# Kernel optimization log

Measured on AMD Instinct MI355X. Metric: run time of the kernel, lower is better.

The kernel has to match this reference:

```python
import jax, jax.numpy as jnp
import numpy as np
import math

D_MODEL = 1024
N_HEADS = 16
D_K = D_MODEL // N_HEADS
B, S = 4, 2048


def setup_inputs() -> dict:
    key = jax.random.key(0)
    ks = jax.random.split(key, 11)
    std = 1.0 / math.sqrt(D_MODEL)
    inp = {
        "query": jax.random.normal(ks[0], (B, S, D_MODEL), dtype=jnp.float32),
        "key_in": jax.random.normal(ks[1], (B, S, D_MODEL), dtype=jnp.float32),
        "value": jax.random.normal(ks[2], (B, S, D_MODEL), dtype=jnp.float32),
        "Wq": jax.random.normal(ks[3], (D_MODEL, D_MODEL), dtype=jnp.float32) * std,
        "bq": jnp.zeros((D_MODEL,), dtype=jnp.float32),
        "Wk": jax.random.normal(ks[4], (D_MODEL, D_MODEL), dtype=jnp.float32) * std,
        "bk": jnp.zeros((D_MODEL,), dtype=jnp.float32),
        "Wv": jax.random.normal(ks[5], (D_MODEL, D_MODEL), dtype=jnp.float32) * std,
        "bv": jnp.zeros((D_MODEL,), dtype=jnp.float32),
        "Wo": jax.random.normal(ks[6], (D_MODEL, D_MODEL), dtype=jnp.float32) * std,
        "bo": jnp.zeros((D_MODEL,), dtype=jnp.float32),
    }
    return inp


def reference(query, key_in, value, Wq, bq, Wk, bk, Wv, bv, Wo, bo):
    b, s, _ = query.shape
    scale = math.sqrt(D_K)
    # projections: nn.Linear computes x @ W.T + b
    Q = (query @ Wq.T + bq).reshape(b, s, N_HEADS, D_K).transpose(0, 2, 1, 3)
    K = (key_in @ Wk.T + bk).reshape(b, s, N_HEADS, D_K).transpose(0, 2, 1, 3)
    V = (value @ Wv.T + bv).reshape(b, s, N_HEADS, D_K).transpose(0, 2, 1, 3)
    # [b, h, s, s]
    scores = jnp.einsum("bhqd,bhkd->bhqk", Q, K) / scale
    causal = jnp.tril(jnp.ones((s, s), dtype=bool))
    scores = jnp.where(causal[None, None, :, :], scores, jnp.float32(-1e9))
    attn = jax.nn.softmax(scores, axis=-1)
    out = jnp.einsum("bhqk,bhkd->bhqd", attn, V)
    out = out.transpose(0, 2, 1, 3).reshape(b, s, D_MODEL)
    return out @ Wo.T + bo
```

## Files before the change

kernel.cpp:

```cpp
#include <hip/hip_runtime.h>
#include <hip/hip_bf16.h>
#include <cstdint>

#define DM   1024
#define NH   16
#define DKK  64
#define BB   4
#define SS   2048

typedef __attribute__((ext_vector_type(8)))  short short8;
typedef __attribute__((ext_vector_type(4)))  float f32x4;
typedef __attribute__((ext_vector_type(16))) float f32x16;

__device__ __forceinline__ unsigned short f2bf(float f) {
    union { float f; uint32_t u; } v; v.f = f;
    uint32_t u = v.u;
    uint32_t r = (u + 0x7FFFu + ((u >> 16) & 1u)) >> 16;
    return (unsigned short)r;
}

__global__ void cvt_w(const float4* __restrict__ wq, const float4* __restrict__ wk,
                      const float4* __restrict__ wv, const float4* __restrict__ wo,
                      ushort4* __restrict__ dst)
{
    const int NW = 262144;
    int i = blockIdx.x * 256 + threadIdx.x;
    int a = i >> 18, off = i & (NW - 1);
    const float4* s = (a == 0 ? wq : a == 1 ? wk : a == 2 ? wv : wo) + off;
    float4 f = *s;
    ushort4 o;
    o.x = f2bf(f.x); o.y = f2bf(f.y); o.z = f2bf(f.z); o.w = f2bf(f.w);
    dst[i] = o;
}

__global__ void gemm_qkv(const float* __restrict__ Aq,
                         const float* __restrict__ Ak,
                         const float* __restrict__ Av,
                         const unsigned short* __restrict__ Wq,
                         const unsigned short* __restrict__ Wk,
                         const unsigned short* __restrict__ Wv,
                         const float* __restrict__ bq,
                         const float* __restrict__ bk,
                         const float* __restrict__ bv,
                         unsigned short* __restrict__ Qo,
                         unsigned short* __restrict__ Ko,
                         unsigned short* __restrict__ Vo,
                         const float qscale)
{
    const int orig = blockIdx.z * 512 + blockIdx.y * 8 + blockIdx.x;
    const int wid  = (orig & 7) * 192 + (orig >> 3);
    const int z    = wid >> 9;
    const int rem  = wid & 511;
    const int brow = (rem >> 3) * 128;
    const int bcol = (rem & 7) * 128;

    const float* A           = (z == 0) ? Aq : (z == 1) ? Ak : Av;
    const unsigned short* Bw = (z == 0) ? Wq : (z == 1) ? Wk : Wv;
    const float* bias        = (z == 0) ? bq : (z == 1) ? bk : bv;

    __shared__ unsigned short lA[128 * 64];
    __shared__ unsigned short lB[128 * 64];
    const int tid = threadIdx.x;
    const int w = tid >> 6, l = tid & 63;
    const int wr = (w >> 1) * 64, wc = (w & 1) * 64;
    const int lrow = l & 15;
    const int lk = (l >> 4) * 8;
    const int sr = l >> 3;
    const int sc = (l & 7) * 8;
    f32x4 acc[4][4] = {};

    for (int k0 = 0; k0 < 1024; k0 += 64) {
#pragma unroll
        for (int i = 0; i < 4; ++i) {
            const int chunk = w * 4 + i;
            const int r = chunk * 8 + sr;
            const unsigned short* gb = Bw + (size_t)(bcol + r) * 1024 + k0 + sc;
            __builtin_amdgcn_global_load_lds((__attribute__((address_space(1))) void*)gb,
                                             (__attribute__((address_space(3))) void*)(lB + chunk * 512),
                                             16, 0, 0);
        }
#pragma unroll
        for (int i = 0; i < 4; ++i) {
            const int chunk = w * 4 + i;
            const int r = chunk * 8 + sr;
            const float* ga = A + (size_t)(brow + r) * 1024 + k0 + sc;
            float4 f0 = *(const float4*)(ga);
            float4 f1 = *(const float4*)(ga + 4);
            union { uint32_t u[4]; short8 s8; } c;
            asm("v_cvt_pk_bf16_f32 %0, %1, %2" : "=v"(c.u[0]) : "v"(f0.x), "v"(f0.y));
            asm("v_cvt_pk_bf16_f32 %0, %1, %2" : "=v"(c.u[1]) : "v"(f0.z), "v"(f0.w));
            asm("v_cvt_pk_bf16_f32 %0, %1, %2" : "=v"(c.u[2]) : "v"(f1.x), "v"(f1.y));
            asm("v_cvt_pk_bf16_f32 %0, %1, %2" : "=v"(c.u[3]) : "v"(f1.z), "v"(f1.w));
            *(short8*)((char*)lA + chunk * 1024 + sr * 128 + sc * 2) = c.s8;
        }
        asm volatile("s_waitcnt vmcnt(0)" ::: "memory");
        __syncthreads();
#pragma unroll
        for (int kk = 0; kk < 2; ++kk) {
            short8 af[4], bfr[4];
#pragma unroll
            for (int m = 0; m < 4; ++m)
                af[m] = *(const short8*)(lA + (wr + m * 16 + lrow) * 64 + kk * 32 + lk);
#pragma unroll
            for (int n = 0; n < 4; ++n)
                bfr[n] = *(const short8*)(lB + (wc + n * 16 + lrow) * 64 + kk * 32 + lk);
#pragma unroll
            for (int m = 0; m < 4; ++m)
#pragma unroll
                for (int n = 0; n < 4; ++n)
                    acc[m][n] = __builtin_amdgcn_mfma_f32_16x16x32_bf16(af[m], bfr[n], acc[m][n], 0, 0, 0);
        }
        __syncthreads();
    }

    const float ascale = (z == 0) ? qscale : 1.0f;
#pragma unroll
    for (int m = 0; m < 4; ++m) {
#pragma unroll
        for (int n = 0; n < 4; ++n) {
            const int i0 = brow + wr + m * 16 + (l >> 4) * 4;
            const int j  = bcol + wc + n * 16 + lrow;
            const float bj = bias[j];
            const int hh = j >> 6, d = j & 63;
            if (z < 2) {
                unsigned short* Cb = (z == 0) ? Qo : Ko;
#pragma unroll
                for (int t = 0; t < 4; ++t) {
                    const int i = i0 + t;
                    const int b = i >> 11, s = i & 2047;
                    Cb[(((size_t)(b * NH + hh) * SS) + s) * DKK + d] = f2bf((acc[m][n][t] + bj) * ascale);
                }
            } else {
                const int b = i0 >> 11, s0 = i0 & 2047;
                ushort4 pk;
                pk.x = f2bf(acc[m][n][0] + bj);
                pk.y = f2bf(acc[m][n][1] + bj);
                pk.z = f2bf(acc[m][n][2] + bj);
                pk.w = f2bf(acc[m][n][3] + bj);
                *(ushort4*)(Vo + (((size_t)(b * NH + hh) * DKK) + d) * SS + s0) = pk;
            }
        }
    }
}

__global__ void gemm_out(const unsigned short* __restrict__ A,
                         const unsigned short* __restrict__ Bw,
                         const float* __restrict__ bias,
                         float* __restrict__ Cout)
{
    const int orig = blockIdx.y * 8 + blockIdx.x;
    const int wid  = (orig & 7) * 64 + (orig >> 3);
    const int brow = (wid >> 3) * 128;
    const int bcol = (wid & 7) * 128;

    __shared__ unsigned short lA[128 * 64];
    __shared__ unsigned short lB[128 * 64];
    const int tid = threadIdx.x;
    const int w = tid >> 6, l = tid & 63;
    const int wr = (w >> 1) * 64, wc = (w & 1) * 64;
    const int lrow = l & 15;
    const int lk = (l >> 4) * 8;
    const int sr = l >> 3;
    const int sc = (l & 7) * 8;
    f32x4 acc[4][4] = {};

    for (int k0 = 0; k0 < 1024; k0 += 64) {
#pragma unroll
        for (int i = 0; i < 4; ++i) {
            const int chunk = w * 4 + i;
            const int r = chunk * 8 + sr;
            const unsigned short* ga = A  + (size_t)(brow + r) * 1024 + k0 + sc;
            const unsigned short* gb = Bw + (size_t)(bcol + r) * 1024 + k0 + sc;
            __builtin_amdgcn_global_load_lds((__attribute__((address_space(1))) void*)ga,
                                             (__attribute__((address_space(3))) void*)(lA + chunk * 512),
                                             16, 0, 0);
            __builtin_amdgcn_global_load_lds((__attribute__((address_space(1))) void*)gb,
                                             (__attribute__((address_space(3))) void*)(lB + chunk * 512),
                                             16, 0, 0);
        }
        asm volatile("s_waitcnt vmcnt(0)" ::: "memory");
        __syncthreads();
#pragma unroll
        for (int kk = 0; kk < 2; ++kk) {
            short8 af[4], bfr[4];
#pragma unroll
            for (int m = 0; m < 4; ++m)
                af[m] = *(const short8*)(lA + (wr + m * 16 + lrow) * 64 + kk * 32 + lk);
#pragma unroll
            for (int n = 0; n < 4; ++n)
                bfr[n] = *(const short8*)(lB + (wc + n * 16 + lrow) * 64 + kk * 32 + lk);
#pragma unroll
            for (int m = 0; m < 4; ++m)
#pragma unroll
                for (int n = 0; n < 4; ++n)
                    acc[m][n] = __builtin_amdgcn_mfma_f32_16x16x32_bf16(af[m], bfr[n], acc[m][n], 0, 0, 0);
        }
        __syncthreads();
    }

#pragma unroll
    for (int m = 0; m < 4; ++m) {
#pragma unroll
        for (int n = 0; n < 4; ++n) {
            const int i0 = brow + wr + m * 16 + (l >> 4) * 4;
            const int j  = bcol + wc + n * 16 + lrow;
            const float bj = bias[j];
#pragma unroll
            for (int t = 0; t < 4; ++t)
                Cout[(size_t)(i0 + t) * DM + j] = acc[m][n][t] + bj;
        }
    }
}

__global__ __launch_bounds__(256) void attn_kernel(
        const unsigned short* __restrict__ Q,
        const unsigned short* __restrict__ K,
        const unsigned short* __restrict__ Vt,
        unsigned short* __restrict__ AO)
{
    const int flat = blockIdx.y * 16 + blockIdx.x;
    const int r8 = flat & 7, k8 = flat >> 3;
    const int bh = r8 * 8 + (k8 & 7);
    const int qchunk = 15 - (k8 >> 3);
    const int tid = threadIdx.x;
    const int w = tid >> 6, l = tid & 63;
    const int ln = l & 31, h = l >> 5;
    const int qb = qchunk * 128;
    const int q0w = qb + w * 32;

    __shared__ __align__(16) char lK[2][4096];
    __shared__ __align__(16) char lV[2][4096];

    const unsigned short* Qp = Q  + ((size_t)bh * SS + q0w) * DKK;
    const unsigned short* Kp = K  + (size_t)bh * SS * DKK;
    const unsigned short* Vp = Vt + (size_t)bh * DKK * SS;

    const int srow = tid >> 3, scb = tid & 7;
    const int swb = srow * 128 + ((scb * 16) ^ ((srow & 7) << 4));
    const unsigned short* ksrc = Kp + srow * DKK + scb * 8;
    const int vd = (scb < 4) ? srow : (srow + 32);
    const unsigned short* vsrc = Vp + (size_t)vd * SS + (scb & 3) * 8;

    int ka[4], va[4];
#pragma unroll
    for (int ks = 0; ks < 4; ++ks)
        ka[ks] = ln * 128 + ((ks * 32 + h * 16) ^ ((ln & 7) << 4));
#pragma unroll
    for (int c = 0; c < 4; ++c)
        va[c] = ln * 128 + ((c * 32 + h * 16) ^ ((ln & 7) << 4));

    short8 qf[4];
#pragma unroll
    for (int ks = 0; ks < 4; ++ks)
        qf[ks] = *(const short8*)(Qp + (size_t)ln * DKK + ks * 16 + h * 8);

    f32x16 o0 = {}, o1 = {};
    float lsum = 0.f;

    const int Tc = qb / 32;
    const int NT = Tc + 4;

    auto compute = [&](int t, int buf) {
        const char* kb = lK[buf];
        const char* vb = lV[buf];
        short8 kf[4];
#pragma unroll
        for (int ks = 0; ks < 4; ++ks) kf[ks] = *(const short8*)(kb + ka[ks]);

        f32x16 s = {};
        __builtin_amdgcn_s_setprio(1);
#pragma unroll
        for (int ks = 0; ks < 4; ++ks)
            s = __builtin_amdgcn_mfma_f32_32x32x16_bf16(kf[ks], qf[ks], s, 0, 0, 0);
        __builtin_amdgcn_s_setprio(0);

        const bool diag = (t == Tc + w);
#pragma unroll
        for (int r = 0; r < 16; ++r) {
            float e;
            asm("v_exp_f32 %0, %1" : "=v"(e) : "v"(s[r]));
            if (diag) {
                const int crow = (r & 3) + 8 * (r >> 2) + 4 * h;
                e = (crow > ln) ? 0.f : e;
            }
            s[r] = e;
            lsum += e;
        }

        uint32_t pk[8];
#pragma unroll
        for (int i = 0; i < 8; ++i) {
            uint32_t d;
            asm("v_cvt_pk_bf16_f32 %0, %1, %2" : "=v"(d) : "v"(s[2 * i]), "v"(s[2 * i + 1]));
            pk[i] = d;
        }
        asm("v_permlane32_swap_b32 %0, %1" : "+v"(pk[0]), "+v"(pk[2]));
        asm("v_permlane32_swap_b32 %0, %1" : "+v"(pk[1]), "+v"(pk[3]));
        asm("v_permlane32_swap_b32 %0, %1" : "+v"(pk[4]), "+v"(pk[6]));
        asm("v_permlane32_swap_b32 %0, %1" : "+v"(pk[5]), "+v"(pk[7]));

        union Ux { uint32_t u[4]; short8 s8; } pa0, pa1;
        pa0.u[0] = pk[0]; pa0.u[1] = pk[1]; pa0.u[2] = pk[2]; pa0.u[3] = pk[3];
        pa1.u[0] = pk[4]; pa1.u[1] = pk[5]; pa1.u[2] = pk[6]; pa1.u[3] = pk[7];

        short8 vf00 = *(const short8*)(vb + va[0]);
        short8 vf10 = *(const short8*)(vb + va[1]);
        short8 vf01 = *(const short8*)(vb + va[2]);
        short8 vf11 = *(const short8*)(vb + va[3]);

        __builtin_amdgcn_s_setprio(1);
        o0 = __builtin_amdgcn_mfma_f32_32x32x16_bf16(pa0.s8, vf00, o0, 0, 0, 0);
        o0 = __builtin_amdgcn_mfma_f32_32x32x16_bf16(pa1.s8, vf10, o0, 0, 0, 0);
        o1 = __builtin_amdgcn_mfma_f32_32x32x16_bf16(pa0.s8, vf01, o1, 0, 0, 0);
        o1 = __builtin_amdgcn_mfma_f32_32x32x16_bf16(pa1.s8, vf11, o1, 0, 0, 0);
        __builtin_amdgcn_s_setprio(0);
    };

    short8 kA = *(const short8*)(ksrc);
    short8 vA = *(const short8*)(vsrc);
    *(short8*)(&lK[0][swb]) = kA;
    *(short8*)(&lV[0][swb]) = vA;
    kA = *(const short8*)(ksrc + 2048);
    vA = *(const short8*)(vsrc + 32);
    short8 kB = {}, vB = {};
    __syncthreads();

    int t = 0, buf = 0;
    for (;;) {
        if (t + 2 < NT) {
            kB = *(const short8*)(ksrc + (size_t)(t + 2) * 2048);
            vB = *(const short8*)(vsrc + (size_t)(t + 2) * 32);
        }
        if (t <= Tc + w) compute(t, buf);
        if (t + 1 < NT) {
            *(short8*)(&lK[buf ^ 1][swb]) = kA;
            *(short8*)(&lV[buf ^ 1][swb]) = vA;
        }
        __syncthreads();
        buf ^= 1;
        if (++t == NT) break;

        if (t + 2 < NT) {
            kA = *(const short8*)(ksrc + (size_t)(t + 2) * 2048);
            vA = *(const short8*)(vsrc + (size_t)(t + 2) * 32);
        }
        if (t <= Tc + w) compute(t, buf);
        if (t + 1 < NT) {
            *(short8*)(&lK[buf ^ 1][swb]) = kB;
            *(short8*)(&lV[buf ^ 1][swb]) = vB;
        }
        __syncthreads();
        buf ^= 1;
        if (++t == NT) break;
    }

    lsum += __shfl_xor(lsum, 32, 64);
    const float rcp = 1.0f / lsum;

    const int bb = bh >> 4, hh = bh & 15;
#pragma unroll
    for (int r = 0; r < 16; ++r) {
        const int crow = (r & 3) + 8 * (r >> 2) + 4 * h;
        const float rl = __shfl(rcp, crow, 64);
        const size_t row = (size_t)(bb * SS + q0w + crow) * DM + hh * DKK;
        AO[row + ln]      = f2bf(o0[r] * rl);
        AO[row + 32 + ln] = f2bf(o1[r] * rl);
    }
}

extern "C" void kernel_launch(void* const* d_in, const int* in_sizes, int n_in,
                              void* d_out, int out_size, void* d_ws, size_t ws_size,
                              hipStream_t stream)
{
    const float* query  = (const float*)d_in[0];
    const float* key_in = (const float*)d_in[1];
    const float* value  = (const float*)d_in[2];
    const float* Wq = (const float*)d_in[3];
    const float* bq = (const float*)d_in[4];
    const float* Wk = (const float*)d_in[5];
    const float* bk = (const float*)d_in[6];
    const float* Wv = (const float*)d_in[7];
    const float* bv = (const float*)d_in[8];
    const float* Wo = (const float*)d_in[9];
    const float* bo = (const float*)d_in[10];

    const size_t NACT = (size_t)BB * SS * DM;
    const size_t NWT  = (size_t)DM * DM;

    unsigned short* ws  = (unsigned short*)d_ws;
    unsigned short* wqb = ws;
    unsigned short* wkb = wqb + NWT;
    unsigned short* wvb = wkb + NWT;
    unsigned short* wob = wvb + NWT;
    unsigned short* Qb  = wob + NWT;
    unsigned short* Kb  = Qb + NACT;
    unsigned short* Vtb = Kb + NACT;
    unsigned short* AOb = Vtb + NACT;

    const int n4 = (int)(4 * (NWT / 4));
    cvt_w<<<n4 / 256, 256, 0, stream>>>((const float4*)Wq, (const float4*)Wk,
                                        (const float4*)Wv, (const float4*)Wo,
                                        (ushort4*)ws);

    const float QSCALE = 0.125f * 1.44269504088896f;
    dim3 gq(DM / 128, (BB * SS) / 128, 3);
    gemm_qkv<<<gq, 256, 0, stream>>>(query, key_in, value, wqb, wkb, wvb,
                                     bq, bk, bv, Qb, Kb, Vtb, QSCALE);

    attn_kernel<<<dim3(16, 64), 256, 0, stream>>>(Qb, Kb, Vtb, AOb);

    dim3 gg(DM / 128, (BB * SS) / 128);
    gemm_out<<<gg, 256, 0, stream>>>(AOb, wob, bo, (float*)d_out);
}
```

Measured before the change: 175.2 us.

## Software-pipeline QKV GEMM with register-prefetched A, double-buffered B, swizzled LDS

The QKV projection GEMM now prefetches the next K-tile of fp32 activations into registers and the next weight tile into a second LDS buffer while computing the current tile. Raw barriers with partial vmcnt waits and s_setprio replace the full drain. The weight conversion kernel pre-swizzles bf16 weights so LDS reads use an XOR pattern that avoids bank conflicts, and the output GEMM's B reads use the same swizzle. This aims to hide global-load latency and cut LDS bank conflicts, at the cost of more LDS and registers, which may lower occupancy.

```diff
diff --git a/kernel.cpp b/kernel.cpp
--- a/kernel.cpp
+++ b/kernel.cpp
@@ -19,33 +19,37 @@
     return (unsigned short)r;
 }
 
-__global__ void cvt_w(const float4* __restrict__ wq, const float4* __restrict__ wk,
-                      const float4* __restrict__ wv, const float4* __restrict__ wo,
-                      ushort4* __restrict__ dst)
+#define GLL(src, dst) __builtin_amdgcn_global_load_lds(                      \
+        (__attribute__((address_space(1))) void*)(src),                      \
+        (__attribute__((address_space(3))) void*)(dst), 16, 0, 0)
+
+__global__ void cvt_w(const float* __restrict__ wq, const float* __restrict__ wk,
+                      const float* __restrict__ wv, const float* __restrict__ wo,
+                      unsigned short* __restrict__ dst)
 {
-    const int NW = 262144;
     int i = blockIdx.x * 256 + threadIdx.x;
-    int a = i >> 18, off = i & (NW - 1);
-    const float4* s = (a == 0 ? wq : a == 1 ? wk : a == 2 ? wv : wo) + off;
-    float4 f = *s;
-    ushort4 o;
-    o.x = f2bf(f.x); o.y = f2bf(f.y); o.z = f2bf(f.z); o.w = f2bf(f.w);
-    dst[i] = o;
-}
-
-__global__ void gemm_qkv(const float* __restrict__ Aq,
-                         const float* __restrict__ Ak,
-                         const float* __restrict__ Av,
-                         const unsigned short* __restrict__ Wq,
-                         const unsigned short* __restrict__ Wk,
-                         const unsigned short* __restrict__ Wv,
-                         const float* __restrict__ bq,
-                         const float* __restrict__ bk,
-                         const float* __restrict__ bv,
-                         unsigned short* __restrict__ Qo,
-                         unsigned short* __restrict__ Ko,
-                         unsigned short* __restrict__ Vo,
-                         const float qscale)
+    int a = i >> 17;
+    int r = i & 131071;
+    int j = r >> 7, kb = r & 127;
+    int kbs = (kb & ~7) | ((kb ^ j) & 7);
+    const float* s = (a == 0 ? wq : a == 1 ? wk : a == 2 ? wv : wo) + (size_t)j * 1024 + kbs * 8;
+    float4 f0 = *(const float4*)(s);
+    float4 f1 = *(const float4*)(s + 4);
+    union { uint32_t u[4]; short8 s8; } c;
+    asm("v_cvt_pk_bf16_f32 %0, %1, %2" : "=v"(c.u[0]) : "v"(f0.x), "v"(f0.y));
+    asm("v_cvt_pk_bf16_f32 %0, %1, %2" : "=v"(c.u[1]) : "v"(f0.z), "v"(f0.w));
+    asm("v_cvt_pk_bf16_f32 %0, %1, %2" : "=v"(c.u[2]) : "v"(f1.x), "v"(f1.y));
+    asm("v_cvt_pk_bf16_f32 %0, %1, %2" : "=v"(c.u[3]) : "v"(f1.z), "v"(f1.w));
+    *(short8*)(dst + ((size_t)a << 20) + (size_t)j * 1024 + kb * 8) = c.s8;
+}
+
+__global__ __launch_bounds__(256) void gemm_qkv(
+        const float* __restrict__ Aq, const float* __restrict__ Ak, const float* __restrict__ Av,
+        const unsigned short* __restrict__ Wq, const unsigned short* __restrict__ Wk,
+        const unsigned short* __restrict__ Wv,
+        const float* __restrict__ bq, const float* __restrict__ bk, const float* __restrict__ bv,
+        unsigned short* __restrict__ Qo, unsigned short* __restrict__ Ko,
+        unsigned short* __restrict__ Vo, const float qscale)
 {
     const int orig = blockIdx.z * 512 + blockIdx.y * 8 + blockIdx.x;
     const int wid  = (orig & 7) * 192 + (orig >> 3);
@@ -58,59 +62,96 @@
     const unsigned short* Bw = (z == 0) ? Wq : (z == 1) ? Wk : Wv;
     const float* bias        = (z == 0) ? bq : (z == 1) ? bk : bv;
 
-    __shared__ unsigned short lA[128 * 64];
-    __shared__ unsigned short lB[128 * 64];
+    __shared__ __align__(16) unsigned short lA[128 * 64];
+    __shared__ __align__(16) unsigned short lB[2][128 * 64];
+
     const int tid = threadIdx.x;
     const int w = tid >> 6, l = tid & 63;
     const int wr = (w >> 1) * 64, wc = (w & 1) * 64;
     const int lrow = l & 15;
-    const int lk = (l >> 4) * 8;
-    const int sr = l >> 3;
-    const int sc = (l & 7) * 8;
+    const int hi = l >> 4;
+    const int sr = l >> 3, scb = l & 7;
+
+    const float* aga[4];
+    int awb[4];
+#pragma unroll
+    for (int i = 0; i < 4; ++i) {
+        const int chunk = w * 4 + i;
+        const int r = chunk * 8 + sr;
+        aga[i] = A + (size_t)(brow + r) * 1024 + scb * 8;
+        awb[i] = chunk * 1024 + sr * 128 + ((scb ^ sr) << 4);
+    }
+
+    f32x4 areg[4][2];
     f32x4 acc[4][4] = {};
 
-    for (int k0 = 0; k0 < 1024; k0 += 64) {
+#pragma unroll
+    for (int i = 0; i < 4; ++i) {
+        const int chunk = w * 4 + i;
+        const int r = chunk * 8 + sr;
+        GLL(Bw + (size_t)(bcol + r) * 1024 + scb * 8, lB[0] + chunk * 512);
+    }
+#pragma unroll
+    for (int i = 0; i < 4; ++i) {
+        areg[i][0] = *(const f32x4*)(aga[i]);
+        areg[i][1] = *(const f32x4*)(aga[i] + 4);
+    }
+
+    for (int t = 0; t < 16; ++t) {
 #pragma unroll
         for (int i = 0; i < 4; ++i) {
-            const int chunk = w * 4 + i;
-            const int r = chunk * 8 + sr;
-            const unsigned short* gb = Bw + (size_t)(bcol + r) * 1024 + k0 + sc;
-            __builtin_amdgcn_global_load_lds((__attribute__((address_space(1))) void*)gb,
-                                             (__attribute__((address_space(3))) void*)(lB + chunk * 512),
-                                             16, 0, 0);
-        }
-#pragma unroll
-        for (int i = 0; i < 4; ++i) {
-            const int chunk = w * 4 + i;
-            const int r = chunk * 8 + sr;
-            const float* ga = A + (size_t)(brow + r) * 1024 + k0 + sc;
-            float4 f0 = *(const float4*)(ga);
-            float4 f1 = *(const float4*)(ga + 4);
             union { uint32_t u[4]; short8 s8; } c;
-            asm("v_cvt_pk_bf16_f32 %0, %1, %2" : "=v"(c.u[0]) : "v"(f0.x), "v"(f0.y));
-            asm("v_cvt_pk_bf16_f32 %0, %1, %2" : "=v"(c.u[1]) : "v"(f0.z), "v"(f0.w));
-            asm("v_cvt_pk_bf16_f32 %0, %1, %2" : "=v"(c.u[2]) : "v"(f1.x), "v"(f1.y));
-            asm("v_cvt_pk_bf16_f32 %0, %1, %2" : "=v"(c.u[3]) : "v"(f1.z), "v"(f1.w));
-            *(short8*)((char*)lA + chunk * 1024 + sr * 128 + sc * 2) = c.s8;
-        }
-        asm volatile("s_waitcnt vmcnt(0)" ::: "memory");
-        __syncthreads();
+            asm("v_cvt_pk_bf16_f32 %0, %1, %2" : "=v"(c.u[0]) : "v"(areg[i][0][0]), "v"(areg[i][0][1]));
+            asm("v_cvt_pk_bf16_f32 %0, %1, %2" : "=v"(c.u[1]) : "v"(areg[i][0][2]), "v"(areg[i][0][3]));
+            asm("v_cvt_pk_bf16_f32 %0, %1, %2" : "=v"(c.u[2]) : "v"(areg[i][1][0]), "v"(areg[i][1][1]));
+            asm("v_cvt_pk_bf16_f32 %0, %1, %2" : "=v"(c.u[3]) : "v"(areg[i][1][2]), "v"(areg[i][1][3]));
+            *(short8*)((char*)lA + awb[i]) = c.s8;
+        }
+        if (t < 15) {
+            const int k0n = (t + 1) * 64;
+#pragma unroll
+            for (int i = 0; i < 4; ++i) {
+                areg[i][0] = *(const f32x4*)(aga[i] + k0n);
+                areg[i][1] = *(const f32x4*)(aga[i] + k0n + 4);
+            }
+#pragma unroll
+            for (int i = 0; i < 4; ++i) {
+                const int chunk = w * 4 + i;
+                const int r = chunk * 8 + sr;
+                GLL(Bw + (size_t)(bcol + r) * 1024 + k0n + scb * 8, lB[(t + 1) & 1] + chunk * 512);
+            }
+            asm volatile("s_waitcnt vmcnt(12) lgkmcnt(0)" ::: "memory");
+        } else {
+            asm volatile("s_waitcnt vmcnt(0) lgkmcnt(0)" ::: "memory");
+        }
+        __builtin_amdgcn_s_barrier();
+        const unsigned short* lb = lB[t & 1];
+        __builtin_amdgcn_s_setprio(1);
 #pragma unroll
         for (int kk = 0; kk < 2; ++kk) {
-            short8 af[4], bfr[4];
+            short8 af[4], bf[4];
+#pragma unroll
+            for (int m = 0; m < 4; ++m) {
+                const int row = wr + m * 16 + lrow;
+                const int pb = (kk * 4 + hi) ^ (row & 7);
+                af[m] = *(const short8*)((const char*)lA + row * 128 + (pb << 4));
+            }
+#pragma unroll
+            for (int n = 0; n < 4; ++n) {
+                const int row = wc + n * 16 + lrow;
+                const int pb = (kk * 4 + hi) ^ (row & 7);
+                bf[n] = *(const short8*)((const char*)lb + row * 128 + (pb << 4));
+            }
 #pragma unroll
             for (int m = 0; m < 4; ++m)
-                af[m] = *(const short8*)(lA + (wr + m * 16 + lrow) * 64 + kk * 32 + lk);
-#pragma unroll
-            for (int n = 0; n < 4; ++n)
-                bfr[n] = *(const short8*)(lB + (wc + n * 16 + lrow) * 64 + kk * 32 + lk);
-#pragma unroll
-            for (int m = 0; m < 4; ++m)
 #pragma unroll
                 for (int n = 0; n < 4; ++n)
-                    acc[m][n] = __builtin_amdgcn_mfma_f32_16x16x32_bf16(af[m], bfr[n], acc[m][n], 0, 0, 0);
-        }
-        __syncthreads();
+                    acc[m][n] = __builtin_amdgcn_mfma_f32_16x16x32_bf16(af[m], bf[n], acc[m][n], 0, 0, 0);
+        }
+        __builtin_amdgcn_s_setprio(0);
+        asm volatile("" ::: "memory");
+        __builtin_amdgcn_s_barrier();
+        asm volatile("" ::: "memory");
     }
 
     const float ascale = (z == 0) ? qscale : 1.0f;
@@ -159,7 +200,8 @@
     const int w = tid >> 6, l = tid & 63;
     const int wr = (w >> 1) * 64, wc = (w & 1) * 64;
     const int lrow = l & 15;
-    const int lk = (l >> 4) * 8;
+    const int hi = l >> 4;
+    const int lk = hi * 8;
     const int sr = l >> 3;
     const int sc = (l & 7) * 8;
     f32x4 acc[4][4] = {};
@@ -169,14 +211,8 @@
         for (int i = 0; i < 4; ++i) {
             const int chunk = w * 4 + i;
             const int r = chunk * 8 + sr;
-            const unsigned short* ga = A  + (size_t)(brow + r) * 1024 + k0 + sc;
-            const unsigned short* gb = Bw + (size_t)(bcol + r) * 1024 + k0 + sc;
-            __builtin_amdgcn_global_load_lds((__attribute__((address_space(1))) void*)ga,
-                                             (__attribute__((address_space(3))) void*)(lA + chunk * 512),
-                                             16, 0, 0);
-            __builtin_amdgcn_global_load_lds((__attribute__((address_space(1))) void*)gb,
-                                             (__attribute__((address_space(3))) void*)(lB + chunk * 512),
-                                             16, 0, 0);
+            GLL(A  + (size_t)(brow + r) * 1024 + k0 + sc, lA + chunk * 512);
+            GLL(Bw + (size_t)(bcol + r) * 1024 + k0 + sc, lB + chunk * 512);
         }
         asm volatile("s_waitcnt vmcnt(0)" ::: "memory");
         __syncthreads();
@@ -187,8 +223,11 @@
             for (int m = 0; m < 4; ++m)
                 af[m] = *(const short8*)(lA + (wr + m * 16 + lrow) * 64 + kk * 32 + lk);
 #pragma unroll
-            for (int n = 0; n < 4; ++n)
-                bfr[n] = *(const short8*)(lB + (wc + n * 16 + lrow) * 64 + kk * 32 + lk);
+            for (int n = 0; n < 4; ++n) {
+                const int row = wc + n * 16 + lrow;
+                const int pb = (kk * 4 + hi) ^ (row & 7);
+                bfr[n] = *(const short8*)((const char*)lB + row * 128 + (pb << 4));
+            }
 #pragma unroll
             for (int m = 0; m < 4; ++m)
 #pragma unroll
@@ -397,10 +436,7 @@
     unsigned short* Vtb = Kb + NACT;
     unsigned short* AOb = Vtb + NACT;
 
-    const int n4 = (int)(4 * (NWT / 4));
-    cvt_w<<<n4 / 256, 256, 0, stream>>>((const float4*)Wq, (const float4*)Wk,
-                                        (const float4*)Wv, (const float4*)Wo,
-                                        (ushort4*)ws);
+    cvt_w<<<2048, 256, 0, stream>>>(Wq, Wk, Wv, Wo, ws);
 
     const float QSCALE = 0.125f * 1.44269504088896f;
     dim3 gq(DM / 128, (BB * SS) / 128, 3);
```

Result: faster. 166.6 us (-4.9%).
